# Optimization experiments

Measured on AMD Instinct MI355X. Metric: run time of the kernel, lower is better.

The kernel has to match this reference:

```python
import jax, jax.numpy as jnp
import numpy as np

B, T, D_IN, D_OUT = 4, 2048, 1024, 1024


def setup_inputs() -> dict:
    key = jax.random.key(0)
    k0, k1, k2, k3 = jax.random.split(key, 4)
    token_embed = jax.random.normal(k0, (B, T, D_IN), dtype=jnp.float32)
    # torch Linear weight is [out, in]; store transposed [in, out] for x @ W
    Wq = jax.random.normal(k1, (D_IN, D_OUT), dtype=jnp.float32) * (1.0 / np.sqrt(D_IN))
    Wk = jax.random.normal(k2, (D_IN, D_OUT), dtype=jnp.float32) * (1.0 / np.sqrt(D_IN))
    Wv = jax.random.normal(k3, (D_IN, D_OUT), dtype=jnp.float32) * (1.0 / np.sqrt(D_IN))
    return {"token_embed": token_embed, "Wq": Wq, "Wk": Wk, "Wv": Wv}


def reference(token_embed, Wq, Wk, Wv):
    # token_embed: [B, T, d_in]
    num_token = token_embed.shape[1]
    q = jnp.einsum("btd,de->bte", token_embed, Wq)  # [B, T, d_out]
    k = jnp.einsum("btd,de->bte", token_embed, Wk)
    v = jnp.einsum("btd,de->bte", token_embed, Wv)
    scores = jnp.einsum("bqe,bke->bqk", q, k)  # [B, T, T]
    # causal mask: strictly-upper-triangular positions set to -inf
    causal = jnp.triu(jnp.ones((num_token, num_token), dtype=bool), k=1)
    scores = jnp.where(causal[None, :, :], -jnp.inf, scores)
    # NOTE: faithful to source bug: scale by sqrt(seq_len) (keys.shape[1]), not sqrt(d_out)
    scale = jnp.asarray(num_token, dtype=scores.dtype) ** 0.5
    attn = jax.nn.softmax(scores / scale, axis=-1)
    # dropout prob is 0 -> identity
    context = jnp.einsum("bqk,bke->bqe", attn, v)  # [B, T, d_out]
    return context
```

## Files before the change

kernel.cpp:

```cpp
#include <hip/hip_runtime.h>
#include <cstdint>
#include <cstddef>
#include <math.h>


typedef __attribute__((ext_vector_type(4))) float f32x4;
typedef __attribute__((ext_vector_type(8))) short s16x8;

#define AS1(p) ((const __attribute__((address_space(1))) void*)(p))
#define AS3(p) ((__attribute__((address_space(3))) void*)(p))
#define BARRIER() asm volatile("s_barrier" ::: "memory")
#define W8 asm volatile("s_waitcnt vmcnt(8)" ::: "memory")
#define W4 asm volatile("s_waitcnt vmcnt(4)" ::: "memory")
#define W0 asm volatile("s_waitcnt vmcnt(0)" ::: "memory")
#define WNONE ((void)0)
#define NOISSUE ((void)0)

static __device__ __forceinline__ unsigned short f2bf(float x) {
  unsigned int u = __float_as_uint(x);
  unsigned int r = u + 0x7FFFu + ((u >> 16) & 1u);
  return (unsigned short)(r >> 16);
}
static __device__ __forceinline__ float bf2f(unsigned short h) {
  return __uint_as_float(((unsigned int)h) << 16);
}

__global__ __launch_bounds__(256) void k_cvt(const float* __restrict__ X,
                                             const float* __restrict__ W0p,
                                             const float* __restrict__ W1p,
                                             const float* __restrict__ W2p,
                                             unsigned short* __restrict__ Xb,
                                             unsigned short* __restrict__ Wt) {
  __shared__ float tile[64][65];
  const int bx = blockIdx.x;
  if (bx < 4096) {
    size_t i = ((size_t)bx * 256 + threadIdx.x) * 8;
    float4 a = *(const float4*)(X + i);
    float4 b = *(const float4*)(X + i + 4);
    union { unsigned short us[8]; uint4 v; } o;
    o.us[0] = f2bf(a.x); o.us[1] = f2bf(a.y); o.us[2] = f2bf(a.z); o.us[3] = f2bf(a.w);
    o.us[4] = f2bf(b.x); o.us[5] = f2bf(b.y); o.us[6] = f2bf(b.z); o.us[7] = f2bf(b.w);
    *(uint4*)(Xb + i) = o.v;
    return;
  }
  const int bx2 = bx - 4096;
  const int z = bx2 >> 8, t = bx2 & 255;
  const float* W = z == 0 ? W0p : (z == 1 ? W1p : W2p);
  unsigned short* dst = Wt + (size_t)z * 1048576;
  const int k0 = (t >> 4) * 64, n0 = (t & 15) * 64;
  const int tr = threadIdx.x >> 4, tc = (threadIdx.x & 15) * 4;
  for (int i = 0; i < 4; ++i) {
    int r = tr + i * 16;
    float4 v = *(const float4*)(W + (size_t)(k0 + r) * 1024 + n0 + tc);
    tile[r][tc + 0] = v.x; tile[r][tc + 1] = v.y;
    tile[r][tc + 2] = v.z; tile[r][tc + 3] = v.w;
  }
  __syncthreads();
  for (int i = 0; i < 4; ++i) {
    int r = tr + i * 16;
    ushort4 o;
    o.x = f2bf(tile[tc + 0][r]); o.y = f2bf(tile[tc + 1][r]);
    o.z = f2bf(tile[tc + 2][r]); o.w = f2bf(tile[tc + 3][r]);
    *(ushort4*)(dst + (size_t)(n0 + r) * 1024 + k0 + tc) = o;
  }
}

static __device__ __forceinline__ void stage2(const char* src, size_t ld128, char* dst) {
  __builtin_amdgcn_global_load_lds(AS1(src), AS3(dst), 16, 0, 0);
  __builtin_amdgcn_global_load_lds(AS1(src + ld128), AS3(dst + 8192), 16, 0, 0);
}

template <class FA, class FB>
static __device__ __forceinline__ void core256(const char* __restrict__ As,
                                               const char* __restrict__ Bs,
                                               size_t ldA128, size_t ldB128,
                                               FA offA, FB offB,
                                               int nkt, char* smem, f32x4 (&acc)[8][4]) {
  const int tid = threadIdx.x, w = tid >> 6, lane = tid & 63;
  const int lr = lane & 15, lq = lane >> 4;
  const int wm = (w >> 2) * 128, wn = (w & 3) * 64;
  char* ldsA = smem + w * 1024;
  char* ldsB = smem + 65536 + w * 1024;
  s16x8 aA[4], aB[4], bA[4], bB[4];

#define STG_A(t, h) stage2(As + offA((t), (h)), ldA128, ldsA + (((t) & 1) * 2 + (h)) * 16384)
#define STG_B(t, h) stage2(Bs + offB((t), (h)), ldB128, ldsB + (((t) & 1) * 2 + (h)) * 16384)
#define RD_A(buf, h, r) (*(const s16x8*)(smem + ((buf) * 2 + (h)) * 16384 + (r) * 64 + ((lq ^ (((r) >> 1) & 3)) << 4)))
#define RD_B(buf, h, r) (*(const s16x8*)(smem + 65536 + ((buf) * 2 + (h)) * 16384 + (r) * 64 + ((lq ^ (((r) >> 1) & 3)) << 4)))
#define RD_ALO(dst, buf, h) \
  _Pragma("unroll") for (int i = 0; i < 4; ++i) dst[i] = RD_A(buf, h, wm + i * 16 + lr);
#define RD_AHI(dst, buf, h) \
  _Pragma("unroll") for (int i = 0; i < 4; ++i) dst[i] = RD_A(buf, h, wm + 64 + i * 16 + lr);
#define RD_BF(dst, buf, h) \
  _Pragma("unroll") for (int c = 0; c < 4; ++c) dst[c] = RD_B(buf, h, wn + c * 16 + lr);
#define ISS_H1(T) do { STG_A((T) + 1, 1); STG_B((T) + 1, 1); } while (0)
#define ISS_H0(T) do { STG_A((T) + 2, 0); STG_B((T) + 2, 0); } while (0)
#define MM(AF, BF, base) \
  __builtin_amdgcn_s_setprio(1); \
  _Pragma("unroll") for (int i = 0; i < 4; ++i) \
  _Pragma("unroll") for (int c = 0; c < 4; ++c) \
    acc[(base) + i][c] = __builtin_amdgcn_mfma_f32_16x16x32_bf16(AF[i], BF[c], acc[(base) + i][c], 0, 0, 0); \
  __builtin_amdgcn_s_setprio(0);
#define TILE(T, ISS0, ISS2, WT0, WT2) { \
    const int _b = (T) & 1; \
    RD_AHI(aB, _b, 0); ISS0; BARRIER(); MM(aA, bA, 0); WT0; BARRIER(); \
    RD_ALO(aA, _b, 1); RD_BF(bB, _b, 1); BARRIER(); MM(aB, bA, 4); BARRIER(); \
    RD_AHI(aB, _b, 1); ISS2; BARRIER(); MM(aA, bB, 0); WT2; BARRIER(); \
    RD_ALO(aA, 1 - _b, 0); RD_BF(bA, 1 - _b, 0); BARRIER(); MM(aB, bB, 4); BARRIER(); \
  }

  STG_A(0, 0); STG_B(0, 0);
  STG_A(0, 1); STG_B(0, 1);
  STG_A(1, 0); STG_B(1, 0);
  W8; BARRIER();
  RD_ALO(aA, 0, 0); RD_BF(bA, 0, 0);

  int t = 0;
  for (; t + 2 < nkt; ++t) TILE(t, ISS_H1(t), ISS_H0(t), W8, W8)
  TILE(t, ISS_H1(t), NOISSUE, W8, W4)
  ++t;
  TILE(t, NOISSUE, NOISSUE, W0, WNONE)

#undef STG_A
#undef STG_B
#undef RD_A
#undef RD_B
#undef RD_ALO
#undef RD_AHI
#undef RD_BF
#undef ISS_H1
#undef ISS_H0
#undef MM
#undef TILE
}

struct OffLinear {
  __device__ __forceinline__ size_t operator()(int t, int h) const {
    return (size_t)t * 128 + (size_t)h * 64;
  }
};
struct OffTriK {
  int k0;
  __device__ __forceinline__ size_t operator()(int t, int h) const {
    int g = k0 + t;
    return (size_t)(g >> 2) * 131072 + (size_t)(g & 3) * 128 + (size_t)h * 64;
  }
};
struct OffLinK {
  int k0;
  __device__ __forceinline__ size_t operator()(int t, int h) const {
    return (size_t)(k0 + t) * 128 + (size_t)h * 64;
  }
};

static __device__ __forceinline__ void lane_src(int& rowl, int& slot) {
  const int tid = threadIdx.x, w = tid >> 6, lane = tid & 63;
  rowl = w * 16 + (lane >> 2);
  slot = (lane & 3) ^ ((rowl >> 1) & 3);
}

__global__ __launch_bounds__(512, 2) void k_qk(const unsigned short* __restrict__ Xb,
                                               const unsigned short* __restrict__ Wt,
                                               unsigned short* __restrict__ Qm,
                                               unsigned short* __restrict__ Km) {
  __shared__ char smem[131072];
  const int by = blockIdx.y, z = by >> 2, q = by & 3, bx = blockIdx.x;
  const int m0 = bx * 256, n0 = q * 256;
  const char* A = (const char*)(Xb + (size_t)m0 * 1024);
  const char* B = (const char*)(Wt + (size_t)z * 1048576 + (size_t)n0 * 1024);
  int rowl, slot; lane_src(rowl, slot);
  const size_t lo = (size_t)rowl * 2048 + slot * 16;
  f32x4 acc[8][4];
#pragma unroll
  for (int i = 0; i < 8; ++i)
#pragma unroll
    for (int c = 0; c < 4; ++c) acc[i][c] = (f32x4){0.f, 0.f, 0.f, 0.f};
  core256(A + lo, B + lo, (size_t)128 * 2048, (size_t)128 * 2048,
          OffLinear{}, OffLinear{}, 16, smem, acc);
  unsigned short* C = z == 0 ? Qm : Km;
  const int tid = threadIdx.x, w = tid >> 6, lane = tid & 63;
  const int lr = lane & 15, lq = lane >> 4;
  const int wm = (w >> 2) * 128, wn = (w & 3) * 64;
#pragma unroll
  for (int fr = 0; fr < 8; ++fr)
#pragma unroll
    for (int fc = 0; fc < 4; ++fc)
#pragma unroll
      for (int i = 0; i < 4; ++i) {
        int row = m0 + wm + fr * 16 + lq * 4 + i;
        int col = n0 + wn + fc * 16 + lr;
        C[(size_t)row * 1024 + col] = f2bf(acc[fr][fc][i]);
      }
}

__global__ __launch_bounds__(512, 2) void k_v(const unsigned short* __restrict__ Xb,
                                              const unsigned short* __restrict__ Wt,
                                              unsigned short* __restrict__ Vt) {
  __shared__ char smem[131072];
  const int x = blockIdx.x;
  const int m0 = (x & 3) * 256, n0 = (x >> 2) * 256;
  const char* A = (const char*)(Wt + (size_t)2 * 1048576 + (size_t)m0 * 1024);
  const char* B = (const char*)(Xb + (size_t)n0 * 1024);
  int rowl, slot; lane_src(rowl, slot);
  const size_t lo = (size_t)rowl * 2048 + slot * 16;
  f32x4 acc[8][4];
#pragma unroll
  for (int a = 0; a < 8; ++a)
#pragma unroll
    for (int c = 0; c < 4; ++c) acc[a][c] = (f32x4){0.f, 0.f, 0.f, 0.f};
  core256(A + lo, B + lo, (size_t)128 * 2048, (size_t)128 * 2048,
          OffLinear{}, OffLinear{}, 16, smem, acc);
  const int tid = threadIdx.x, w = tid >> 6, lane = tid & 63;
  const int lr = lane & 15, lq = lane >> 4;
  const int wm = (w >> 2) * 128, wn = (w & 3) * 64;
#pragma unroll
  for (int fr = 0; fr < 8; ++fr)
#pragma unroll
    for (int fc = 0; fc < 4; ++fc)
#pragma unroll
      for (int i = 0; i < 4; ++i) {
        int row = m0 + wm + fr * 16 + lq * 4 + i;
        int col = n0 + wn + fc * 16 + lr;
        Vt[((size_t)(col >> 11) * 1024 + row) * 2048 + (col & 2047)] = f2bf(acc[fr][fc][i]);
      }
}

__global__ __launch_bounds__(512, 2) void k_sg(const unsigned short* __restrict__ Qm,
                                               const unsigned short* __restrict__ Km,
                                               unsigned short* __restrict__ S) {
  __shared__ char smem[131072];
  const int id = blockIdx.x;
  int i = 0;
  while ((i + 1) * (i + 2) / 2 <= id) ++i;
  const int j = id - i * (i + 1) / 2;
  const int b = blockIdx.y;
  const int m0 = i * 256, n0 = j * 256;
  int rowl, slot; lane_src(rowl, slot);
  const size_t lo = (size_t)rowl * 2048 + slot * 16;
  f32x4 acc[8][4];
#pragma unroll
  for (int a = 0; a < 8; ++a)
#pragma unroll
    for (int c = 0; c < 4; ++c) acc[a][c] = (f32x4){0.f, 0.f, 0.f, 0.f};
  core256((const char*)(Qm + ((size_t)b * 2048 + m0) * 1024) + lo,
          (const char*)(Km + ((size_t)b * 2048 + n0) * 1024) + lo,
          (size_t)128 * 2048, (size_t)128 * 2048, OffLinear{}, OffLinear{}, 16, smem, acc);
  const float SCALE = 0.022097086912079608f;
  const int tid = threadIdx.x, w = tid >> 6, lane = tid & 63;
  const int lr = lane & 15, lq = lane >> 4;
  const int wm = (w >> 2) * 128, wn = (w & 3) * 64;
  unsigned short* tb = S + (((size_t)(b * 36 + id)) << 16);
#pragma unroll
  for (int fr = 0; fr < 8; ++fr)
#pragma unroll
    for (int fc = 0; fc < 4; ++fc)
#pragma unroll
      for (int i2 = 0; i2 < 4; ++i2) {
        int rl = wm + fr * 16 + lq * 4 + i2;
        int cl = wn + fc * 16 + lr;
        tb[(size_t)rl * 256 + cl] = f2bf(acc[fr][fc][i2] * SCALE);
      }
}

__global__ __launch_bounds__(256) void k_softmax(unsigned short* __restrict__ S) {
  const int tid = threadIdx.x, w = tid >> 6, lane = tid & 63;
  const int row = blockIdx.x * 4 + w;
  const int b = row >> 11, q = row & 2047;
  const int i = q >> 8, ntl = i + 1, rowL = q & 255;
  unsigned short* base = S + (((size_t)(b * 36 + (i * (i + 1)) / 2)) << 16)
                           + (size_t)rowL * 256 + lane * 4;
  float v[8][4];
#pragma unroll
  for (int t = 0; t < 8; ++t) {
    if (t < ntl) {
      ushort4 x = *(const ushort4*)(base + (size_t)t * 65536);
      int c0 = t * 256 + lane * 4;
      v[t][0] = (c0 + 0 <= q) ? bf2f(x.x) : -INFINITY;
      v[t][1] = (c0 + 1 <= q) ? bf2f(x.y) : -INFINITY;
      v[t][2] = (c0 + 2 <= q) ? bf2f(x.z) : -INFINITY;
      v[t][3] = (c0 + 3 <= q) ? bf2f(x.w) : -INFINITY;
    } else {
      v[t][0] = v[t][1] = v[t][2] = v[t][3] = -INFINITY;
    }
  }
  float m = -INFINITY;
#pragma unroll
  for (int t = 0; t < 8; ++t)
#pragma unroll
    for (int jj = 0; jj < 4; ++jj) m = fmaxf(m, v[t][jj]);
  for (int off = 32; off; off >>= 1) m = fmaxf(m, __shfl_xor(m, off));
  float s = 0.f;
#pragma unroll
  for (int t = 0; t < 8; ++t)
#pragma unroll
    for (int jj = 0; jj < 4; ++jj) { v[t][jj] = __expf(v[t][jj] - m); s += v[t][jj]; }
  for (int off = 32; off; off >>= 1) s += __shfl_xor(s, off);
  const float inv = 1.f / s;
#pragma unroll
  for (int t = 0; t < 8; ++t)
    if (t < ntl) {
      ushort4 o;
      o.x = f2bf(v[t][0] * inv); o.y = f2bf(v[t][1] * inv);
      o.z = f2bf(v[t][2] * inv); o.w = f2bf(v[t][3] * inv);
      *(ushort4*)(base + (size_t)t * 65536) = o;
    }
}

__device__ const int pvi[15] = {2, 5, 5, 7, 7, 4, 4, 6, 7, 6, 6, 1, 3, 3, 0};
__device__ const int pvk[15] = {0, 0, 12, 0, 11, 0, 10, 0, 22, 10, 19, 0, 0, 8, 0};
__device__ const int pvn[15] = {12, 12, 12, 11, 11, 10, 10, 10, 10, 9, 9, 8, 8, 8, 4};
__device__ const int pvp[15] = {-1, -1, 2, -1, 5, -1, 1, -1, 6, 3, 4, -1, -1, 0, -1};

__global__ __launch_bounds__(512, 2) void k_pv(const unsigned short* __restrict__ P,
                                               const unsigned short* __restrict__ Vt,
                                               float* __restrict__ out,
                                               float* __restrict__ part) {
  __shared__ char smem[131072];
  const int cx = blockIdx.x % 15;
  const int panel = blockIdx.x / 15;
  const int nt = panel & 3, b = panel >> 2;
  const int i = pvi[cx], k0 = pvk[cx], nkt = pvn[cx], psl = pvp[cx];
  const char* Pb = (const char*)P + (((size_t)(b * 36 + (i * (i + 1)) / 2)) << 17);
  int rowl, slot; lane_src(rowl, slot);
  const char* Asrc = Pb + (size_t)rowl * 512 + slot * 16;
  const char* Bsrc = (const char*)Vt + ((size_t)(b * 1024 + nt * 256 + rowl)) * 4096 + slot * 16;
  f32x4 acc[8][4];
#pragma unroll
  for (int a = 0; a < 8; ++a)
#pragma unroll
    for (int c = 0; c < 4; ++c) acc[a][c] = (f32x4){0.f, 0.f, 0.f, 0.f};
  core256(Asrc, Bsrc, (size_t)128 * 512, (size_t)128 * 4096,
          OffTriK{k0}, OffLinK{k0}, nkt, smem, acc);
  const int tid = threadIdx.x, w = tid >> 6, lane = tid & 63;
  const int lr = lane & 15, lq = lane >> 4;
  const int wm = (w >> 2) * 128, wn = (w & 3) * 64;
  if (psl < 0) {
#pragma unroll
    for (int fr = 0; fr < 8; ++fr)
#pragma unroll
      for (int fc = 0; fc < 4; ++fc)
#pragma unroll
        for (int i2 = 0; i2 < 4; ++i2) {
          int orow = i * 256 + wm + fr * 16 + lq * 4 + i2;
          int col = nt * 256 + wn + fc * 16 + lr;
          out[((size_t)b * 2048 + orow) * 1024 + col] = acc[fr][fc][i2];
        }
  } else {
    float* pt = part + ((size_t)(panel * 7 + psl)) * 65536;
#pragma unroll
    for (int fr = 0; fr < 8; ++fr)
#pragma unroll
      for (int fc = 0; fc < 4; ++fc)
#pragma unroll
        for (int i2 = 0; i2 < 4; ++i2) {
          int rl = wm + fr * 16 + lq * 4 + i2;
          int cl = wn + fc * 16 + lr;
          pt[(size_t)rl * 256 + cl] = acc[fr][fc][i2];
        }
  }
}

__global__ __launch_bounds__(256) void k_fix(float* __restrict__ out,
                                             const float* __restrict__ part) {
  const size_t e = ((size_t)blockIdx.x * 256 + threadIdx.x) * 4;
  const int b = (int)(e / 1310720);
  const int rem = (int)(e % 1310720);
  const int row = 768 + (rem >> 10);
  const int col = rem & 1023;
  const int i = row >> 8;
  const int nt = col >> 8;
  const int base4[5] = {0, 1, 2, 3, 5};
  const int cnt4[5] = {1, 1, 1, 2, 2};
  const int sb = base4[i - 3], cnt = cnt4[i - 3];
  const float* pt = part + ((size_t)((b * 4 + nt) * 7 + sb)) * 65536
                         + (size_t)(row & 255) * 256 + (col & 255);
  float* op = out + ((size_t)b * 2048 + row) * 1024 + col;
  float4 o = *(const float4*)op;
  float4 p0 = *(const float4*)pt;
  o.x += p0.x; o.y += p0.y; o.z += p0.z; o.w += p0.w;
  if (cnt == 2) {
    float4 p1 = *(const float4*)(pt + 65536);
    o.x += p1.x; o.y += p1.y; o.z += p1.z; o.w += p1.w;
  }
  *(float4*)op = o;
}

extern "C" void kernel_launch(void* const* d_in, const int* in_sizes, int n_in,
                              void* d_out, int out_size, void* d_ws, size_t ws_size,
                              hipStream_t stream) {
  const float* X  = (const float*)d_in[0];
  const float* W0p = (const float*)d_in[1];
  const float* W1p = (const float*)d_in[2];
  const float* W2p = (const float*)d_in[3];
  float* out = (float*)d_out;
  char* ws = (char*)d_ws;
  unsigned short* Xb = (unsigned short*)ws;
  unsigned short* Wt = (unsigned short*)(ws + (size_t)16777216);
  unsigned short* Qm = (unsigned short*)(ws + (size_t)23068672);
  unsigned short* Km = (unsigned short*)(ws + (size_t)39845888);
  unsigned short* Vt = (unsigned short*)(ws + (size_t)56623104);
  unsigned short* Sb = (unsigned short*)ws;
  float* Pp = (float*)(ws + (size_t)23068672);
  (void)in_sizes; (void)n_in; (void)out_size; (void)ws_size;

  hipLaunchKernelGGL(k_cvt, dim3(4864), dim3(256), 0, stream, X, W0p, W1p, W2p, Xb, Wt);
  hipLaunchKernelGGL(k_qk, dim3(32, 8), dim3(512), 0, stream, Xb, Wt, Qm, Km);
  hipLaunchKernelGGL(k_v, dim3(128), dim3(512), 0, stream, Xb, Wt, Vt);
  hipLaunchKernelGGL(k_sg, dim3(36, 4), dim3(512), 0, stream, Qm, Km, Sb);
  hipLaunchKernelGGL(k_softmax, dim3(2048), dim3(256), 0, stream, Sb);
  hipLaunchKernelGGL(k_pv, dim3(240), dim3(512), 0, stream, Sb, Vt, out, Pp);
  hipLaunchKernelGGL(k_fix, dim3(5120), dim3(256), 0, stream, out, Pp);
}
```

Before: 173.2 us.

## Restructure GEMM core into eight-phase pipeline and rebalance PV work split

Measured after the change: 164.5 us. 5.0% less time.

```diff
diff --git a/kernel.cpp b/kernel.cpp
--- a/kernel.cpp
+++ b/kernel.cpp
@@ -13,6 +13,8 @@
 #define W8 asm volatile("s_waitcnt vmcnt(8)" ::: "memory")
 #define W4 asm volatile("s_waitcnt vmcnt(4)" ::: "memory")
 #define W0 asm volatile("s_waitcnt vmcnt(0)" ::: "memory")
+#define LGKM0 do { asm volatile("s_waitcnt lgkmcnt(0)" ::: "memory"); \
+                   __builtin_amdgcn_sched_barrier(0); } while (0)
 #define WNONE ((void)0)
 #define NOISSUE ((void)0)
 
@@ -81,57 +83,64 @@
   const int wm = (w >> 2) * 128, wn = (w & 3) * 64;
   char* ldsA = smem + w * 1024;
   char* ldsB = smem + 65536 + w * 1024;
-  s16x8 aA[4], aB[4], bA[4], bB[4];
+  s16x8 afA[4], afB[4], bfA[4], bfB[4];
 
 #define STG_A(t, h) stage2(As + offA((t), (h)), ldA128, ldsA + (((t) & 1) * 2 + (h)) * 16384)
 #define STG_B(t, h) stage2(Bs + offB((t), (h)), ldB128, ldsB + (((t) & 1) * 2 + (h)) * 16384)
 #define RD_A(buf, h, r) (*(const s16x8*)(smem + ((buf) * 2 + (h)) * 16384 + (r) * 64 + ((lq ^ (((r) >> 1) & 3)) << 4)))
 #define RD_B(buf, h, r) (*(const s16x8*)(smem + 65536 + ((buf) * 2 + (h)) * 16384 + (r) * 64 + ((lq ^ (((r) >> 1) & 3)) << 4)))
-#define RD_ALO(dst, buf, h) \
-  _Pragma("unroll") for (int i = 0; i < 4; ++i) dst[i] = RD_A(buf, h, wm + i * 16 + lr);
-#define RD_AHI(dst, buf, h) \
-  _Pragma("unroll") for (int i = 0; i < 4; ++i) dst[i] = RD_A(buf, h, wm + 64 + i * 16 + lr);
-#define RD_BF(dst, buf, h) \
-  _Pragma("unroll") for (int c = 0; c < 4; ++c) dst[c] = RD_B(buf, h, wn + c * 16 + lr);
-#define ISS_H1(T) do { STG_A((T) + 1, 1); STG_B((T) + 1, 1); } while (0)
-#define ISS_H0(T) do { STG_A((T) + 2, 0); STG_B((T) + 2, 0); } while (0)
-#define MM(AF, BF, base) \
-  __builtin_amdgcn_s_setprio(1); \
+#define MMQ(AF, BF, base) \
   _Pragma("unroll") for (int i = 0; i < 4; ++i) \
   _Pragma("unroll") for (int c = 0; c < 4; ++c) \
-    acc[(base) + i][c] = __builtin_amdgcn_mfma_f32_16x16x32_bf16(AF[i], BF[c], acc[(base) + i][c], 0, 0, 0); \
-  __builtin_amdgcn_s_setprio(0);
-#define TILE(T, ISS0, ISS2, WT0, WT2) { \
-    const int _b = (T) & 1; \
-    RD_AHI(aB, _b, 0); ISS0; BARRIER(); MM(aA, bA, 0); WT0; BARRIER(); \
-    RD_ALO(aA, _b, 1); RD_BF(bB, _b, 1); BARRIER(); MM(aB, bA, 4); BARRIER(); \
-    RD_AHI(aB, _b, 1); ISS2; BARRIER(); MM(aA, bB, 0); WT2; BARRIER(); \
-    RD_ALO(aA, 1 - _b, 0); RD_BF(bA, 1 - _b, 0); BARRIER(); MM(aB, bB, 4); BARRIER(); \
-  }
+    acc[(base) + i][c] = __builtin_amdgcn_mfma_f32_16x16x32_bf16(AF[i], BF[c], acc[(base) + i][c], 0, 0, 0)
+#define PH_E(tt, hh, AFD, BFD, STG, WAIT) \
+  _Pragma("unroll") for (int i = 0; i < 4; ++i) AFD[i] = RD_A((tt) & 1, hh, wm + i * 16 + lr); \
+  _Pragma("unroll") for (int c = 0; c < 4; ++c) BFD[c] = RD_B((tt) & 1, hh, wn + c * 16 + lr); \
+  STG; WAIT; BARRIER(); LGKM0; \
+  __builtin_amdgcn_s_setprio(1); MMQ(AFD, BFD, 0); __builtin_amdgcn_s_setprio(0); \
+  BARRIER();
+#define PH_O(tt, hh, AFD, BFU, STG, WAIT) \
+  _Pragma("unroll") for (int i = 0; i < 4; ++i) AFD[i] = RD_A((tt) & 1, hh, wm + 64 + i * 16 + lr); \
+  STG; WAIT; BARRIER(); LGKM0; \
+  __builtin_amdgcn_s_setprio(1); MMQ(AFD, BFU, 4); __builtin_amdgcn_s_setprio(0); \
+  BARRIER();
 
   STG_A(0, 0); STG_B(0, 0);
   STG_A(0, 1); STG_B(0, 1);
   STG_A(1, 0); STG_B(1, 0);
   W8; BARRIER();
-  RD_ALO(aA, 0, 0); RD_BF(bA, 0, 0);
-
-  int t = 0;
-  for (; t + 2 < nkt; ++t) TILE(t, ISS_H1(t), ISS_H0(t), W8, W8)
-  TILE(t, ISS_H1(t), NOISSUE, W8, W4)
-  ++t;
-  TILE(t, NOISSUE, NOISSUE, W0, WNONE)
+
+  const int niter = nkt >> 1;
+  for (int I = 0; I < niter - 1; ++I) {
+    const int t0 = 2 * I, t1 = 2 * I + 1;
+    PH_E(t0, 0, afA, bfA, STG_A(t1, 1),     WNONE)
+    PH_O(t0, 0, afB, bfA, STG_B(t1, 1),     W8)
+    PH_E(t0, 1, afA, bfB, STG_A(t0 + 2, 0), WNONE)
+    PH_O(t0, 1, afB, bfB, STG_B(t0 + 2, 0), W8)
+    PH_E(t1, 0, afA, bfA, STG_A(t0 + 2, 1), WNONE)
+    PH_O(t1, 0, afB, bfA, STG_B(t0 + 2, 1), W8)
+    PH_E(t1, 1, afA, bfB, STG_A(t1 + 2, 0), WNONE)
+    PH_O(t1, 1, afB, bfB, STG_B(t1 + 2, 0), W8)
+  }
+  {
+    const int t0 = nkt - 2, t1 = nkt - 1;
+    PH_E(t0, 0, afA, bfA, STG_A(t1, 1), WNONE)
+    PH_O(t0, 0, afB, bfA, STG_B(t1, 1), W8)
+    PH_E(t0, 1, afA, bfB, NOISSUE,      WNONE)
+    PH_O(t0, 1, afB, bfB, NOISSUE,      W4)
+    PH_E(t1, 0, afA, bfA, NOISSUE,      WNONE)
+    PH_O(t1, 0, afB, bfA, NOISSUE,      W0)
+    PH_E(t1, 1, afA, bfB, NOISSUE,      WNONE)
+    PH_O(t1, 1, afB, bfB, NOISSUE,      WNONE)
+  }
 
 #undef STG_A
 #undef STG_B
 #undef RD_A
 #undef RD_B
-#undef RD_ALO
-#undef RD_AHI
-#undef RD_BF
-#undef ISS_H1
-#undef ISS_H0
-#undef MM
-#undef TILE
+#undef MMQ
+#undef PH_E
+#undef PH_O
 }
 
 struct OffLinear {
@@ -306,10 +315,10 @@
     }
 }
 
-__device__ const int pvi[15] = {2, 5, 5, 7, 7, 4, 4, 6, 7, 6, 6, 1, 3, 3, 0};
-__device__ const int pvk[15] = {0, 0, 12, 0, 11, 0, 10, 0, 22, 10, 19, 0, 0, 8, 0};
-__device__ const int pvn[15] = {12, 12, 12, 11, 11, 10, 10, 10, 10, 9, 9, 8, 8, 8, 4};
-__device__ const int pvp[15] = {-1, -1, 2, -1, 5, -1, 1, -1, 6, 3, 4, -1, -1, 0, -1};
+__device__ const int pvi[15] = {2, 5, 5, 7, 7, 4, 4, 6, 6, 1, 3, 3, 6, 7, 0};
+__device__ const int pvk[15] = {0, 0, 12, 0, 12, 0, 10, 0, 10, 0, 0, 8, 20, 24, 0};
+__device__ const int pvn[15] = {12, 12, 12, 12, 12, 10, 10, 10, 10, 8, 8, 8, 8, 8, 4};
+__device__ const int pvp[15] = {-1, -1, 2, -1, 5, -1, 1, -1, 3, -1, -1, 0, 4, 6, -1};
 
 __global__ __launch_bounds__(512, 2) void k_pv(const unsigned short* __restrict__ P,
                                                const unsigned short* __restrict__ Vt,
```
